# Kernel optimization log

Measured on AMD Instinct MI355X. Metric: run time of the kernel, lower is better.

The kernel has to match this reference:

```python
import jax, jax.numpy as jnp
import numpy as np

PAD = [(1, 1), (1, 1), (1, 1)]
DN = ('NCDHW', 'OIDHW', 'NCDHW')


def conv3d(x, w):
    # x: [B,Ci,D,H,W], w: [Co,Ci,3,3,3], stride 1, pad 1 (BasicConv3d, bn=False, bias=False)
    return jax.lax.conv_general_dilated(x, w, (1, 1, 1), PAD, dimension_numbers=DN)


def deconv3d(x, w):
    # torch ConvTranspose3d weight [Ci,Co,3,3,3], stride 1, pad 1 == conv with spatially flipped kernel
    wf = jnp.flip(w, axis=(2, 3, 4)).transpose(1, 0, 2, 3, 4)
    return conv3d(x, wf)


def sru_dir(X, Wx, F, R, reverse):
    # SRU linear recurrence over the spectral axis (dim 2).
    # t=0: C = 1 - f_0 (faithful to SRUconvLayer's Ct-is-None branch)
    # t>0: C = f*C + (1-f)*Wx ;  h = r*C + (1-r)*x
    mt = lambda a: jnp.moveaxis(a, 2, 0)  # [T,B,C,H,W]
    x, w, f, r = mt(X), mt(Wx), mt(F), mt(R)
    if reverse:
        x, w, f, r = x[::-1], w[::-1], f[::-1], r[::-1]
    C0 = 1.0 - f[0]
    h0 = r[0] * C0 + (1.0 - r[0]) * x[0]

    def step(C, inp):
        x_, w_, f_, r_ = inp
        Cn = f_ * C + (1.0 - f_) * w_
        return Cn, r_ * Cn + (1.0 - r_) * x_

    _, hs = jax.lax.scan(step, C0, (x[1:], w[1:], f[1:], r[1:]))
    h = jnp.concatenate([h0[None], hs], axis=0)
    if reverse:
        h = h[::-1]
    return jnp.moveaxis(h, 0, 2)


def do_sru(x, w, deconv=False):
    # DoSRUconv: 6-way gate split, bidirectional scan (ft/rt forward, ft2/rt2 backward), sum
    g = deconv3d(x, w) if deconv else conv3d(x, w)
    Wx, ft, ft2, rt, rt2, X = jnp.split(g, 6, axis=1)
    Wx = jnp.tanh(Wx)
    X = jnp.tanh(X)  # act == 'tanh'
    ft, ft2, rt, rt2 = (jax.nn.sigmoid(a) for a in (ft, ft2, rt, rt2))
    return sru_dir(X, Wx, ft, rt, False) + sru_dir(X, Wx, ft2, rt2, True)


def si_sru(x, w, reverse, deconv=False):
    # SiSRUconv: 4-way gate split, single-direction scan
    g = deconv3d(x, w) if deconv else conv3d(x, w)
    Wx, ft, rt, X = jnp.split(g, 4, axis=1)
    return sru_dir(jnp.tanh(X), jnp.tanh(Wx), jax.nn.sigmoid(ft), jax.nn.sigmoid(rt), reverse)


def nssnn_forward(x, w_head, w_e0, w_e1, w_d0, w_d1, w_tail):
    h = do_sru(x, w_head)                                 # head: 1 -> 16, bidirectional
    e0 = si_sru(h, w_e0, reverse=False)                   # encoder: 16 -> 32 (alt direction)
    e1 = si_sru(e0, w_e1, reverse=True)                   # encoder: 32 -> 64
    d0 = si_sru(e1, w_d0, reverse=False, deconv=True) + e0  # decoder: 64 -> 32, skip add
    d1 = si_sru(d0, w_d1, reverse=True, deconv=True) + h    # decoder: 32 -> 16, skip add
    out = do_sru(d1, w_tail, deconv=True)                 # tail: 16 -> 1, bidirectional
    return out + x                                        # global residual


def setup_inputs() -> dict:
    key = jax.random.key(0)
    ks = jax.random.split(key, 7)
    B, Cin, Ch, D, H, W = 1, 1, 16, 31, 96, 96
    s = 0.05
    x = jax.random.normal(ks[0], (B, Cin, D, H, W), dtype=jnp.float32)
    w_head = jax.random.normal(ks[1], (6 * Ch, Cin, 3, 3, 3), dtype=jnp.float32) * s
    w_e0 = jax.random.normal(ks[2], (4 * 2 * Ch, Ch, 3, 3, 3), dtype=jnp.float32) * s
    w_e1 = jax.random.normal(ks[3], (4 * 4 * Ch, 2 * Ch, 3, 3, 3), dtype=jnp.float32) * s
    # ConvTranspose3d weights: [Cin, Cout, 3,3,3]
    w_d0 = jax.random.normal(ks[4], (4 * Ch, 4 * 2 * Ch, 3, 3, 3), dtype=jnp.float32) * s
    w_d1 = jax.random.normal(ks[5], (2 * Ch, 4 * Ch, 3, 3, 3), dtype=jnp.float32) * s
    w_tail = jax.random.normal(ks[6], (Ch, 6 * Cin, 3, 3, 3), dtype=jnp.float32) * s
    return {"x": x, "w_head": w_head, "w_e0": w_e0, "w_e1": w_e1,
            "w_d0": w_d0, "w_d1": w_d1, "w_tail": w_tail}


def reference(x, w_head, w_e0, w_e1, w_d0, w_d1, w_tail):
    return nssnn_forward(x, w_head, w_e0, w_e1, w_d0, w_d1, w_tail)
```

## Files before the change

### kernel.cpp

```cpp
#include <hip/hip_runtime.h>
#include <hip/hip_bf16.h>


#define D_DIM 31
#define H_DIM 96
#define W_DIM 96
#define HW (H_DIM * W_DIM)
#define SVOX (D_DIM * HW)

typedef __hip_bfloat16 bf16;
typedef __attribute__((ext_vector_type(8))) short short8;
typedef __attribute__((ext_vector_type(4))) short short4a;
typedef __attribute__((ext_vector_type(4))) float f32x4;

__device__ __forceinline__ float sigm(float v) { return 1.0f / (1.0f + __expf(-v)); }
__device__ __forceinline__ short f2bs(float v) {
    bf16 h = __float2bfloat16(v);
    return *(short*)&h;
}
__device__ __forceinline__ float bs2f(short s) {
    return __uint_as_float(((unsigned)(unsigned short)s) << 16);
}

template <typename T> __device__ __forceinline__ float ldf(const T* p);
template <> __device__ __forceinline__ float ldf<float>(const float* p) { return *p; }
template <> __device__ __forceinline__ float ldf<bf16>(const bf16* p) {
    return __bfloat162float(*p);
}
template <typename T> __device__ __forceinline__ void stf(T* p, float v);
template <> __device__ __forceinline__ void stf<float>(float* p, float v) { *p = v; }
template <> __device__ __forceinline__ void stf<bf16>(bf16* p, float v) {
    *p = __float2bfloat16(v);
}

#define P8 ((size_t)8 * SVOX)

__global__ __launch_bounds__(256) void wtrans_all_k(const float* __restrict__ w_e0,
                                                    const float* __restrict__ w_e1,
                                                    const float* __restrict__ w_d0,
                                                    const float* __restrict__ w_d1,
                                                    bf16* __restrict__ wt) {
    int i = blockIdx.x * 256 + threadIdx.x;
    if (i >= 608256) return;
    const float* w;
    int j, C_in, C_out_w, Ch, deconv, cip;
    if (i < 110592)      { w = w_e0; j = i;          C_in = 16; C_out_w = 128; Ch = 32; deconv = 0; cip = 32; }
    else if (i < 331776) { w = w_e1; j = i - 110592; C_in = 32; C_out_w = 256; Ch = 64; deconv = 0; cip = 32; }
    else if (i < 552960) { w = w_d0; j = i - 331776; C_in = 64; C_out_w = 128; Ch = 32; deconv = 1; cip = 64; }
    else                 { w = w_d1; j = i - 552960; C_in = 32; C_out_w = 64;  Ch = 16; deconv = 1; cip = 32; }
    int ci = j % cip;
    int r = j / cip;
    int oc_c = r & 31; r >>= 5;
    int kk = r % 27;
    int chunk = r / 27;
    int oc_w = (oc_c >> 3) * Ch + chunk * 8 + (oc_c & 7);
    float v = 0.0f;
    if (ci < C_in)
        v = deconv ? w[((size_t)ci * C_out_w + oc_w) * 27 + (26 - kk)]
                   : w[((size_t)oc_w * C_in + ci) * 27 + kk];
    wt[i] = __float2bfloat16(v);
}

template <int CI32>
__global__ __launch_bounds__(256) void conv_mfma_k(const bf16* __restrict__ x,
                                                   const bf16* __restrict__ wt,
                                                   bf16* __restrict__ g, int C_in) {
    constexpr int RS = 40;
    constexpr int CIP = CI32 * 32;
    __shared__ short row[6 * 98 * RS];

    const int t = threadIdx.x;
    const int lane = t & 63, wave = t >> 6;
    const int l15 = lane & 15, g4 = lane >> 4;
    const int h0 = blockIdx.x * 4, d = blockIdx.y;
    const short* xs = (const short*)x;

    f32x4 acc[6][2];
#pragma unroll
    for (int m = 0; m < 6; ++m)
#pragma unroll
        for (int n = 0; n < 2; ++n) acc[m][n] = (f32x4){0.f, 0.f, 0.f, 0.f};

    for (int kd = 0; kd < 3; ++kd) {
        const int dd = d + kd - 1;
        if ((unsigned)dd >= D_DIM) continue;
        for (int cb = 0; cb < CI32; ++cb) {
            __syncthreads();
            for (int i = t; i < 98 * 6 * 4; i += 256) {
                int wp = i % 98;
                int j = i / 98;
                int hl = j % 6;
                int cg = j / 6;
                int hh = h0 + hl - 1;
                int gw = wp - 1;
                const int cblk = cb * 4 + cg;
                short8 v = {0, 0, 0, 0, 0, 0, 0, 0};
                if ((unsigned)hh < H_DIM && (unsigned)gw < W_DIM && cblk * 8 < C_in)
                    v = *(const short8*)(xs + (size_t)cblk * P8 +
                                         ((size_t)dd * HW + hh * W_DIM + gw) * 8);
                *(short8*)(row + ((size_t)hl * 98 + wp) * RS + cg * 8) = v;
            }
            __syncthreads();

            const bf16* wa = wt + (size_t)l15 * CIP + cb * 32 + g4 * 8;
#pragma unroll
            for (int kh = 0; kh < 3; ++kh) {
#pragma unroll
                for (int kw = 0; kw < 3; ++kw) {
                    const int kk = (kd * 3 + kh) * 3 + kw;
                    const size_t arow = (size_t)kk * 32 * CIP;
                    short8 a0 = *(const short8*)(wa + arow);
                    short8 a1 = *(const short8*)(wa + arow + (size_t)16 * CIP);
                    const int boff = ((wave + kh) * 98 + l15 + kw) * RS + g4 * 8;
#pragma unroll
                    for (int m = 0; m < 6; ++m) {
                        short8 b = *(const short8*)(row + boff + (m * 16) * RS);
                        acc[m][0] = __builtin_amdgcn_mfma_f32_16x16x32_bf16(a0, b, acc[m][0], 0, 0, 0);
                        acc[m][1] = __builtin_amdgcn_mfma_f32_16x16x32_bf16(a1, b, acc[m][1], 0, 0, 0);
                    }
                }
            }
        }
    }

    const int hy = h0 + wave;
    short* gs = (short*)g;
#pragma unroll
    for (int m = 0; m < 6; ++m) {
        const int wx = m * 16 + l15;
        const size_t dhw = (size_t)d * HW + hy * W_DIM + wx;
#pragma unroll
        for (int n = 0; n < 2; ++n) {
            const int gate = n * 2 + (g4 >> 1);
            const bool th = (gate == 0 || gate == 3);
            short4a pack;
#pragma unroll
            for (int r = 0; r < 4; ++r) {
                float a = acc[m][n][r];
                pack[r] = f2bs(th ? tanhf(a) : sigm(a));
            }
            *(short4a*)(gs + (size_t)gate * P8 + dhw * 8 + (g4 & 1) * 4) = pack;
        }
    }
}

__global__ __launch_bounds__(256) void head_conv_k(const float* __restrict__ x,
                                                   const float* __restrict__ w,
                                                   bf16* __restrict__ g, int c0) {
    __shared__ float tile[3][34][36];
    __shared__ float wsh[8 * 27];

    const int t = threadIdx.x;
    const int lx = t & 15;
    const int ly = t >> 4;
    const int tbx = (blockIdx.x % 3) * 32;
    const int tby = (blockIdx.x / 3) * 32;
    const int d = blockIdx.y;
    const int gidx = blockIdx.z;
    const int ocw0 = gidx * 16 + c0;

    if (t < 8 * 27) wsh[t] = w[(ocw0 + t / 27) * 27 + (t % 27)];

    for (int i = t; i < 3 * 34 * 34; i += 256) {
        int dz = i / 1156;
        int rem = i - dz * 1156;
        int r = rem / 34;
        int c = rem - r * 34;
        int gd = d + dz - 1;
        int gy = tby + r - 1;
        int gx = tbx + c - 1;
        float v = 0.0f;
        if ((unsigned)gd < D_DIM && (unsigned)gy < H_DIM && (unsigned)gx < W_DIM)
            v = x[((size_t)gd * H_DIM + gy) * W_DIM + gx];
        tile[dz][r][c] = v;
    }
    __syncthreads();

    float acc[8][4];
#pragma unroll
    for (int o = 0; o < 8; ++o)
#pragma unroll
        for (int p = 0; p < 4; ++p) acc[o][p] = 0.0f;

#pragma unroll
    for (int kd = 0; kd < 3; ++kd)
#pragma unroll
        for (int kh = 0; kh < 3; ++kh) {
            float wv[8][3];
#pragma unroll
            for (int o = 0; o < 8; ++o)
#pragma unroll
                for (int kw = 0; kw < 3; ++kw)
                    wv[o][kw] = wsh[o * 27 + (kd * 3 + kh) * 3 + kw];
            const int r0 = ly * 2 + kh;
            float v0[4], v1[4];
#pragma unroll
            for (int c = 0; c < 4; ++c) {
                v0[c] = tile[kd][r0][lx * 2 + c];
                v1[c] = tile[kd][r0 + 1][lx * 2 + c];
            }
#pragma unroll
            for (int kw = 0; kw < 3; ++kw)
#pragma unroll
                for (int o = 0; o < 8; ++o) {
                    acc[o][0] = fmaf(v0[kw],     wv[o][kw], acc[o][0]);
                    acc[o][1] = fmaf(v0[kw + 1], wv[o][kw], acc[o][1]);
                    acc[o][2] = fmaf(v1[kw],     wv[o][kw], acc[o][2]);
                    acc[o][3] = fmaf(v1[kw + 1], wv[o][kw], acc[o][3]);
                }
        }

    const bool th = (gidx == 0 || gidx == 5);
    const int hy = tby + ly * 2, wx = tbx + lx * 2;
    short* gs = (short*)g;
#pragma unroll
    for (int p = 0; p < 4; ++p) {
        const int py = hy + (p >> 1), px = wx + (p & 1);
        short8 pack;
#pragma unroll
        for (int o = 0; o < 8; ++o) {
            float a = acc[o][p];
            pack[o] = f2bs(th ? tanhf(a) : sigm(a));
        }
        *(short8*)(gs + (size_t)gidx * P8 + ((size_t)d * HW + py * W_DIM + px) * 8) = pack;
    }
}

__global__ __launch_bounds__(256) void tail_conv_k(const bf16* __restrict__ x,
                                                   const float* __restrict__ w,
                                                   bf16* __restrict__ g) {
    __shared__ short tile[3][18][18][8];
    __shared__ float wsh[8 * 6 * 27];

    const int t = threadIdx.x;
    const int lx = t & 15;
    const int ly = t >> 4;
    const int tbx = (blockIdx.x % 6) * 16;
    const int tby = (blockIdx.x / 6) * 16;
    const int d = blockIdx.y;
    const short* xs = (const short*)x;

    float acc[6] = {0.f, 0.f, 0.f, 0.f, 0.f, 0.f};

    for (int cb = 0; cb < 2; ++cb) {
        __syncthreads();
        for (int i = t; i < 8 * 6 * 27; i += 256) {
            int u = i / 162, rem = i % 162, o = rem / 27, k = rem % 27;
            wsh[i] = w[((cb * 8 + u) * 6 + o) * 27 + (26 - k)];
        }
        for (int i = t; i < 3 * 18 * 18; i += 256) {
            int dz = i / 324;
            int rem = i % 324;
            int r = rem / 18;
            int cc = rem % 18;
            int gd = d + dz - 1;
            int gy = tby + r - 1;
            int gx = tbx + cc - 1;
            short8 v = {0, 0, 0, 0, 0, 0, 0, 0};
            if ((unsigned)gd < D_DIM && (unsigned)gy < H_DIM && (unsigned)gx < W_DIM)
                v = *(const short8*)(xs + (size_t)cb * P8 +
                                     ((size_t)gd * HW + gy * W_DIM + gx) * 8);
            *(short8*)&tile[dz][r][cc][0] = v;
        }
        __syncthreads();

#pragma unroll
        for (int kd = 0; kd < 3; ++kd)
#pragma unroll
            for (int kh = 0; kh < 3; ++kh)
#pragma unroll
                for (int kw = 0; kw < 3; ++kw) {
                    short8 tv = *(short8*)&tile[kd][ly + kh][lx + kw][0];
                    const int k = (kd * 3 + kh) * 3 + kw;
#pragma unroll
                    for (int u = 0; u < 8; ++u) {
                        float xv = bs2f(tv[u]);
#pragma unroll
                        for (int o = 0; o < 6; ++o)
                            acc[o] = fmaf(xv, wsh[(u * 6 + o) * 27 + k], acc[o]);
                    }
                }
    }

    const size_t dhw = (size_t)d * HW + (tby + ly) * W_DIM + (tbx + lx);
#pragma unroll
    for (int o = 0; o < 6; ++o) {
        const bool th = (o == 0 || o == 5);
        stf(g + (size_t)o * SVOX + dhw, th ? tanhf(acc[o]) : sigm(acc[o]));
    }
}

template <int REV>
__global__ __launch_bounds__(256) void si_sru_scan_k(const bf16* __restrict__ g,
                                                     const bf16* __restrict__ resid,
                                                     bf16* __restrict__ out, int outblk) {
    const int idx = blockIdx.x * 256 + threadIdx.x;
    const int c = idx & 7;
    const size_t hw = (size_t)(idx >> 3);

    const bf16* oW = g;
    const bf16* oF = g + P8;
    const bf16* oR = g + 2 * P8;
    const bf16* oX = g + 3 * P8;
    const size_t ob = (size_t)outblk * P8;

    float C = 0.0f;
#pragma unroll
    for (int i = 0; i < D_DIM; ++i) {
        const int d = REV ? (D_DIM - 1 - i) : i;
        const size_t off = ((size_t)d * HW + hw) * 8 + c;
        float f = ldf(oF + off);
        float r = ldf(oR + off);
        float xv = ldf(oX + off);
        float wv = ldf(oW + off);
        C = (i == 0) ? (1.0f - f) : (f * C + (1.0f - f) * wv);
        float hv = r * C + (1.0f - r) * xv;
        float o = hv + (resid ? ldf(resid + ob + off) : 0.0f);
        stf(out + ob + off, o);
    }
}

__global__ __launch_bounds__(256) void do_sru_scan_k(const bf16* __restrict__ g,
                                                     bf16* __restrict__ out, int outblk) {
    const int idx = blockIdx.x * 256 + threadIdx.x;
    const int c = idx & 7;
    const size_t hw = (size_t)(idx >> 3);
    const size_t ob = (size_t)outblk * P8;

    float hbuf[D_DIM];
    float C = 0.0f;
#pragma unroll
    for (int d = 0; d < D_DIM; ++d) {
        const size_t off = ((size_t)d * HW + hw) * 8 + c;
        float f = ldf(g + P8 + off);
        float r = ldf(g + 3 * P8 + off);
        float xv = ldf(g + 5 * P8 + off);
        float wv = ldf(g + off);
        C = (d == 0) ? (1.0f - f) : (f * C + (1.0f - f) * wv);
        hbuf[d] = r * C + (1.0f - r) * xv;
    }
#pragma unroll
    for (int i = 0; i < D_DIM; ++i) {
        const int d = D_DIM - 1 - i;
        const size_t off = ((size_t)d * HW + hw) * 8 + c;
        float f = ldf(g + 2 * P8 + off);
        float r = ldf(g + 4 * P8 + off);
        float xv = ldf(g + 5 * P8 + off);
        float wv = ldf(g + off);
        C = (i == 0) ? (1.0f - f) : (f * C + (1.0f - f) * wv);
        hbuf[d] += r * C + (1.0f - r) * xv;
    }
#pragma unroll
    for (int d = 0; d < D_DIM; ++d)
        stf(out + ob + ((size_t)d * HW + hw) * 8 + c, hbuf[d]);
}

__global__ __launch_bounds__(256) void do_sru_final_k(const bf16* __restrict__ g,
                                                      const float* __restrict__ x,
                                                      float* __restrict__ out) {
    const size_t hw = (size_t)(blockIdx.x * 256 + threadIdx.x);

    float hbuf[D_DIM];
    float C = 0.0f;
#pragma unroll
    for (int d = 0; d < D_DIM; ++d) {
        const size_t off = (size_t)d * HW + hw;
        float f = ldf(g + SVOX + off);
        float r = ldf(g + 3 * (size_t)SVOX + off);
        float xv = ldf(g + 5 * (size_t)SVOX + off);
        float wv = ldf(g + off);
        C = (d == 0) ? (1.0f - f) : (f * C + (1.0f - f) * wv);
        hbuf[d] = r * C + (1.0f - r) * xv;
    }
#pragma unroll
    for (int i = 0; i < D_DIM; ++i) {
        const int d = D_DIM - 1 - i;
        const size_t off = (size_t)d * HW + hw;
        float f = ldf(g + 2 * (size_t)SVOX + off);
        float r = ldf(g + 4 * (size_t)SVOX + off);
        float xv = ldf(g + 5 * (size_t)SVOX + off);
        float wv = ldf(g + off);
        C = (i == 0) ? (1.0f - f) : (f * C + (1.0f - f) * wv);
        hbuf[d] += r * C + (1.0f - r) * xv + x[off];
    }
#pragma unroll
    for (int d = 0; d < D_DIM; ++d) out[(size_t)d * HW + hw] = hbuf[d];
}

extern "C" void kernel_launch(void* const* d_in, const int* in_sizes, int n_in,
                              void* d_out, int out_size, void* d_ws, size_t ws_size,
                              hipStream_t stream) {
    const float* x      = (const float*)d_in[0];
    const float* w_head = (const float*)d_in[1];
    const float* w_e0   = (const float*)d_in[2];
    const float* w_e1   = (const float*)d_in[3];
    const float* w_d0   = (const float*)d_in[4];
    const float* w_d1   = (const float*)d_in[5];
    const float* w_tail = (const float*)d_in[6];
    float* out = (float*)d_out;

    bf16* g  = (bf16*)d_ws;
    bf16* wt = g + (size_t)32 * SVOX;
    bf16* H  = g + (size_t)48 * SVOX;
    bf16* E0 = H + (size_t)16 * SVOX;
    bf16* E1 = E0 + (size_t)32 * SVOX;
    bf16* D0 = E0;
    bf16* D1 = E1;

    dim3 blk(256);
    const dim3 sg8(8 * 36);
    const dim3 mg(H_DIM / 4, D_DIM);

    for (int c0 = 0; c0 < 16; c0 += 8) {
        head_conv_k<<<dim3(9, 31, 6), blk, 0, stream>>>(x, w_head, g, c0);
        do_sru_scan_k<<<sg8, blk, 0, stream>>>(g, H, c0 >> 3);
    }
    wtrans_all_k<<<dim3((608256 + 255) / 256), blk, 0, stream>>>(w_e0, w_e1, w_d0, w_d1, wt);

    for (int c = 0; c < 4; ++c) {
        conv_mfma_k<1><<<mg, blk, 0, stream>>>(H, wt + (size_t)c * 27648, g, 16);
        si_sru_scan_k<0><<<sg8, blk, 0, stream>>>(g, (const bf16*)nullptr, E0, c);
    }
    for (int c = 0; c < 8; ++c) {
        conv_mfma_k<1><<<mg, blk, 0, stream>>>(E0, wt + 110592 + (size_t)c * 27648, g, 32);
        si_sru_scan_k<1><<<sg8, blk, 0, stream>>>(g, (const bf16*)nullptr, E1, c);
    }
    for (int c = 0; c < 4; ++c) {
        conv_mfma_k<2><<<mg, blk, 0, stream>>>(E1, wt + 331776 + (size_t)c * 55296, g, 64);
        si_sru_scan_k<0><<<sg8, blk, 0, stream>>>(g, E0, D0, c);
    }
    for (int c = 0; c < 2; ++c) {
        conv_mfma_k<1><<<mg, blk, 0, stream>>>(D0, wt + 552960 + (size_t)c * 27648, g, 32);
        si_sru_scan_k<1><<<sg8, blk, 0, stream>>>(g, H, D1, c);
    }
    tail_conv_k<<<dim3(36, 31), blk, 0, stream>>>(D1, w_tail, g);
    do_sru_final_k<<<dim3(36), blk, 0, stream>>>(g, x, out);
}
```

Before: 1.293 ms.

## Route tail conv through MFMA kernel, batch head conv/scan, pad LDS rows

Replaces the scalar FMA tail convolution with the MFMA conv kernel, templated on tile count and epilogue, using a pre-transposed flipped tail weight block added to the weight transform. Head conv and bidirectional scan now run once over all 16 channels instead of two launches each, which needs a reworked workspace layout. LDS row stride drops from 40 to 34 shorts to cut bank conflicts, though short8 loads at that stride may lose 16-byte alignment. The tail MFMA path wastes most of its output tile because only 6 of 16 channels are real.

```diff
diff --git a/kernel.cpp b/kernel.cpp
--- a/kernel.cpp
+++ b/kernel.cpp
@@ -39,9 +39,22 @@
                                                     const float* __restrict__ w_e1,
                                                     const float* __restrict__ w_d0,
                                                     const float* __restrict__ w_d1,
+                                                    const float* __restrict__ w_tail,
                                                     bf16* __restrict__ wt) {
     int i = blockIdx.x * 256 + threadIdx.x;
-    if (i >= 608256) return;
+    if (i >= 635904) return;
+    if (i >= 608256) {
+        int j = i - 608256;
+        int ci = j % 32;
+        int r = j / 32;
+        int oc_c = r & 31;
+        int kk = (r >> 5) % 27;
+        float v = 0.0f;
+        if (ci < 16 && oc_c < 6)
+            v = w_tail[(ci * 6 + oc_c) * 27 + (26 - kk)];
+        wt[i] = __float2bfloat16(v);
+        return;
+    }
     const float* w;
     int j, C_in, C_out_w, Ch, deconv, cip;
     if (i < 110592)      { w = w_e0; j = i;          C_in = 16; C_out_w = 128; Ch = 32; deconv = 0; cip = 32; }
@@ -61,11 +74,11 @@
     wt[i] = __float2bfloat16(v);
 }
 
-template <int CI32>
+template <int CI32, int NT, int EPI>
 __global__ __launch_bounds__(256) void conv_mfma_k(const bf16* __restrict__ x,
                                                    const bf16* __restrict__ wt,
                                                    bf16* __restrict__ g, int C_in) {
-    constexpr int RS = 40;
+    constexpr int RS = 34;
     constexpr int CIP = CI32 * 32;
     __shared__ short row[6 * 98 * RS];
 
@@ -75,11 +88,11 @@
     const int h0 = blockIdx.x * 4, d = blockIdx.y;
     const short* xs = (const short*)x;
 
-    f32x4 acc[6][2];
+    f32x4 acc[6][NT];
 #pragma unroll
     for (int m = 0; m < 6; ++m)
 #pragma unroll
-        for (int n = 0; n < 2; ++n) acc[m][n] = (f32x4){0.f, 0.f, 0.f, 0.f};
+        for (int n = 0; n < NT; ++n) acc[m][n] = (f32x4){0.f, 0.f, 0.f, 0.f};
 
     for (int kd = 0; kd < 3; ++kd) {
         const int dd = d + kd - 1;
@@ -110,13 +123,15 @@
                     const int kk = (kd * 3 + kh) * 3 + kw;
                     const size_t arow = (size_t)kk * 32 * CIP;
                     short8 a0 = *(const short8*)(wa + arow);
-                    short8 a1 = *(const short8*)(wa + arow + (size_t)16 * CIP);
+                    short8 a1;
+                    if (NT == 2) a1 = *(const short8*)(wa + arow + (size_t)16 * CIP);
                     const int boff = ((wave + kh) * 98 + l15 + kw) * RS + g4 * 8;
 #pragma unroll
                     for (int m = 0; m < 6; ++m) {
                         short8 b = *(const short8*)(row + boff + (m * 16) * RS);
                         acc[m][0] = __builtin_amdgcn_mfma_f32_16x16x32_bf16(a0, b, acc[m][0], 0, 0, 0);
-                        acc[m][1] = __builtin_amdgcn_mfma_f32_16x16x32_bf16(a1, b, acc[m][1], 0, 0, 0);
+                        if (NT == 2)
+                            acc[m][1] = __builtin_amdgcn_mfma_f32_16x16x32_bf16(a1, b, acc[m][1], 0, 0, 0);
                     }
                 }
             }
@@ -129,24 +144,36 @@
     for (int m = 0; m < 6; ++m) {
         const int wx = m * 16 + l15;
         const size_t dhw = (size_t)d * HW + hy * W_DIM + wx;
-#pragma unroll
-        for (int n = 0; n < 2; ++n) {
-            const int gate = n * 2 + (g4 >> 1);
-            const bool th = (gate == 0 || gate == 3);
-            short4a pack;
+        if (EPI == 0) {
+#pragma unroll
+            for (int n = 0; n < NT; ++n) {
+                const int gate = n * 2 + (g4 >> 1);
+                const bool th = (gate == 0 || gate == 3);
+                short4a pack;
+#pragma unroll
+                for (int r = 0; r < 4; ++r) {
+                    float a = acc[m][n][r];
+                    pack[r] = f2bs(th ? tanhf(a) : sigm(a));
+                }
+                *(short4a*)(gs + (size_t)gate * P8 + dhw * 8 + (g4 & 1) * 4) = pack;
+            }
+        } else {
 #pragma unroll
             for (int r = 0; r < 4; ++r) {
-                float a = acc[m][n][r];
-                pack[r] = f2bs(th ? tanhf(a) : sigm(a));
-            }
-            *(short4a*)(gs + (size_t)gate * P8 + dhw * 8 + (g4 & 1) * 4) = pack;
+                const int oc = g4 * 4 + r;
+                if (oc < 6) {
+                    float a = acc[m][0][r];
+                    const bool th = (oc == 0 || oc == 5);
+                    stf(g + (size_t)oc * SVOX + dhw, th ? tanhf(a) : sigm(a));
+                }
+            }
         }
     }
 }
 
 __global__ __launch_bounds__(256) void head_conv_k(const float* __restrict__ x,
                                                    const float* __restrict__ w,
-                                                   bf16* __restrict__ g, int c0) {
+                                                   bf16* __restrict__ g) {
     __shared__ float tile[3][34][36];
     __shared__ float wsh[8 * 27];
 
@@ -156,8 +183,9 @@
     const int tbx = (blockIdx.x % 3) * 32;
     const int tby = (blockIdx.x / 3) * 32;
     const int d = blockIdx.y;
-    const int gidx = blockIdx.z;
-    const int ocw0 = gidx * 16 + c0;
+    const int bz = blockIdx.z;
+    const int gate = bz >> 1;
+    const int ocw0 = gate * 16 + (bz & 1) * 8;
 
     if (t < 8 * 27) wsh[t] = w[(ocw0 + t / 27) * 27 + (t % 27)];
 
@@ -210,7 +238,7 @@
                 }
         }
 
-    const bool th = (gidx == 0 || gidx == 5);
+    const bool th = (gate == 0 || gate == 5);
     const int hy = tby + ly * 2, wx = tbx + lx * 2;
     short* gs = (short*)g;
 #pragma unroll
@@ -222,71 +250,7 @@
             float a = acc[o][p];
             pack[o] = f2bs(th ? tanhf(a) : sigm(a));
         }
-        *(short8*)(gs + (size_t)gidx * P8 + ((size_t)d * HW + py * W_DIM + px) * 8) = pack;
-    }
-}
-
-__global__ __launch_bounds__(256) void tail_conv_k(const bf16* __restrict__ x,
-                                                   const float* __restrict__ w,
-                                                   bf16* __restrict__ g) {
-    __shared__ short tile[3][18][18][8];
-    __shared__ float wsh[8 * 6 * 27];
-
-    const int t = threadIdx.x;
-    const int lx = t & 15;
-    const int ly = t >> 4;
-    const int tbx = (blockIdx.x % 6) * 16;
-    const int tby = (blockIdx.x / 6) * 16;
-    const int d = blockIdx.y;
-    const short* xs = (const short*)x;
-
-    float acc[6] = {0.f, 0.f, 0.f, 0.f, 0.f, 0.f};
-
-    for (int cb = 0; cb < 2; ++cb) {
-        __syncthreads();
-        for (int i = t; i < 8 * 6 * 27; i += 256) {
-            int u = i / 162, rem = i % 162, o = rem / 27, k = rem % 27;
-            wsh[i] = w[((cb * 8 + u) * 6 + o) * 27 + (26 - k)];
-        }
-        for (int i = t; i < 3 * 18 * 18; i += 256) {
-            int dz = i / 324;
-            int rem = i % 324;
-            int r = rem / 18;
-            int cc = rem % 18;
-            int gd = d + dz - 1;
-            int gy = tby + r - 1;
-            int gx = tbx + cc - 1;
-            short8 v = {0, 0, 0, 0, 0, 0, 0, 0};
-            if ((unsigned)gd < D_DIM && (unsigned)gy < H_DIM && (unsigned)gx < W_DIM)
-                v = *(const short8*)(xs + (size_t)cb * P8 +
-                                     ((size_t)gd * HW + gy * W_DIM + gx) * 8);
-            *(short8*)&tile[dz][r][cc][0] = v;
-        }
-        __syncthreads();
-
-#pragma unroll
-        for (int kd = 0; kd < 3; ++kd)
-#pragma unroll
-            for (int kh = 0; kh < 3; ++kh)
-#pragma unroll
-                for (int kw = 0; kw < 3; ++kw) {
-                    short8 tv = *(short8*)&tile[kd][ly + kh][lx + kw][0];
-                    const int k = (kd * 3 + kh) * 3 + kw;
-#pragma unroll
-                    for (int u = 0; u < 8; ++u) {
-                        float xv = bs2f(tv[u]);
-#pragma unroll
-                        for (int o = 0; o < 6; ++o)
-                            acc[o] = fmaf(xv, wsh[(u * 6 + o) * 27 + k], acc[o]);
-                    }
-                }
-    }
-
-    const size_t dhw = (size_t)d * HW + (tby + ly) * W_DIM + (tbx + lx);
-#pragma unroll
-    for (int o = 0; o < 6; ++o) {
-        const bool th = (o == 0 || o == 5);
-        stf(g + (size_t)o * SVOX + dhw, th ? tanhf(acc[o]) : sigm(acc[o]));
+        *(short8*)(gs + (size_t)bz * P8 + ((size_t)d * HW + py * W_DIM + px) * 8) = pack;
     }
 }
 
@@ -297,11 +261,6 @@
     const int idx = blockIdx.x * 256 + threadIdx.x;
     const int c = idx & 7;
     const size_t hw = (size_t)(idx >> 3);
-
-    const bf16* oW = g;
-    const bf16* oF = g + P8;
-    const bf16* oR = g + 2 * P8;
-    const bf16* oX = g + 3 * P8;
     const size_t ob = (size_t)outblk * P8;
 
     float C = 0.0f;
@@ -309,10 +268,10 @@
     for (int i = 0; i < D_DIM; ++i) {
         const int d = REV ? (D_DIM - 1 - i) : i;
         const size_t off = ((size_t)d * HW + hw) * 8 + c;
-        float f = ldf(oF + off);
-        float r = ldf(oR + off);
-        float xv = ldf(oX + off);
-        float wv = ldf(oW + off);
+        float f = ldf(g + P8 + off);
+        float r = ldf(g + 2 * P8 + off);
+        float xv = ldf(g + 3 * P8 + off);
+        float wv = ldf(g + off);
         C = (i == 0) ? (1.0f - f) : (f * C + (1.0f - f) * wv);
         float hv = r * C + (1.0f - r) * xv;
         float o = hv + (resid ? ldf(resid + ob + off) : 0.0f);
@@ -321,21 +280,22 @@
 }
 
 __global__ __launch_bounds__(256) void do_sru_scan_k(const bf16* __restrict__ g,
-                                                     bf16* __restrict__ out, int outblk) {
-    const int idx = blockIdx.x * 256 + threadIdx.x;
-    const int c = idx & 7;
-    const size_t hw = (size_t)(idx >> 3);
-    const size_t ob = (size_t)outblk * P8;
+                                                     bf16* __restrict__ out) {
+    const int j = blockIdx.x * 256 + threadIdx.x;
+    const int c = j & 7;
+    const size_t hw = (size_t)(j >> 3);
+    const int chb = blockIdx.y;
+    const bf16* gb = g + (size_t)chb * P8;
 
     float hbuf[D_DIM];
     float C = 0.0f;
 #pragma unroll
     for (int d = 0; d < D_DIM; ++d) {
         const size_t off = ((size_t)d * HW + hw) * 8 + c;
-        float f = ldf(g + P8 + off);
-        float r = ldf(g + 3 * P8 + off);
-        float xv = ldf(g + 5 * P8 + off);
-        float wv = ldf(g + off);
+        float f = ldf(gb + 2 * P8 + off);
+        float r = ldf(gb + 6 * P8 + off);
+        float xv = ldf(gb + 10 * P8 + off);
+        float wv = ldf(gb + off);
         C = (d == 0) ? (1.0f - f) : (f * C + (1.0f - f) * wv);
         hbuf[d] = r * C + (1.0f - r) * xv;
     }
@@ -343,16 +303,16 @@
     for (int i = 0; i < D_DIM; ++i) {
         const int d = D_DIM - 1 - i;
         const size_t off = ((size_t)d * HW + hw) * 8 + c;
-        float f = ldf(g + 2 * P8 + off);
-        float r = ldf(g + 4 * P8 + off);
-        float xv = ldf(g + 5 * P8 + off);
-        float wv = ldf(g + off);
+        float f = ldf(gb + 4 * P8 + off);
+        float r = ldf(gb + 8 * P8 + off);
+        float xv = ldf(gb + 10 * P8 + off);
+        float wv = ldf(gb + off);
         C = (i == 0) ? (1.0f - f) : (f * C + (1.0f - f) * wv);
         hbuf[d] += r * C + (1.0f - r) * xv;
     }
 #pragma unroll
     for (int d = 0; d < D_DIM; ++d)
-        stf(out + ob + ((size_t)d * HW + hw) * 8 + c, hbuf[d]);
+        stf(out + (size_t)chb * P8 + ((size_t)d * HW + hw) * 8 + c, hbuf[d]);
 }
 
 __global__ __launch_bounds__(256) void do_sru_final_k(const bf16* __restrict__ g,
@@ -401,9 +361,9 @@
 
     bf16* g  = (bf16*)d_ws;
     bf16* wt = g + (size_t)32 * SVOX;
-    bf16* H  = g + (size_t)48 * SVOX;
-    bf16* E0 = H + (size_t)16 * SVOX;
-    bf16* E1 = E0 + (size_t)32 * SVOX;
+    bf16* E1 = g + (size_t)48 * SVOX;
+    bf16* E0 = g + (size_t)112 * SVOX;
+    bf16* H  = g + (size_t)144 * SVOX;
     bf16* D0 = E0;
     bf16* D1 = E1;
 
@@ -411,28 +371,26 @@
     const dim3 sg8(8 * 36);
     const dim3 mg(H_DIM / 4, D_DIM);
 
-    for (int c0 = 0; c0 < 16; c0 += 8) {
-        head_conv_k<<<dim3(9, 31, 6), blk, 0, stream>>>(x, w_head, g, c0);
-        do_sru_scan_k<<<sg8, blk, 0, stream>>>(g, H, c0 >> 3);
-    }
-    wtrans_all_k<<<dim3((608256 + 255) / 256), blk, 0, stream>>>(w_e0, w_e1, w_d0, w_d1, wt);
+    head_conv_k<<<dim3(9, 31, 12), blk, 0, stream>>>(x, w_head, g);
+    do_sru_scan_k<<<dim3(288, 2), blk, 0, stream>>>(g, H);
+    wtrans_all_k<<<dim3((635904 + 255) / 256), blk, 0, stream>>>(w_e0, w_e1, w_d0, w_d1, w_tail, wt);
 
     for (int c = 0; c < 4; ++c) {
-        conv_mfma_k<1><<<mg, blk, 0, stream>>>(H, wt + (size_t)c * 27648, g, 16);
+        conv_mfma_k<1, 2, 0><<<mg, blk, 0, stream>>>(H, wt + (size_t)c * 27648, g, 16);
         si_sru_scan_k<0><<<sg8, blk, 0, stream>>>(g, (const bf16*)nullptr, E0, c);
     }
     for (int c = 0; c < 8; ++c) {
-        conv_mfma_k<1><<<mg, blk, 0, stream>>>(E0, wt + 110592 + (size_t)c * 27648, g, 32);
+        conv_mfma_k<1, 2, 0><<<mg, blk, 0, stream>>>(E0, wt + 110592 + (size_t)c * 27648, g, 32);
         si_sru_scan_k<1><<<sg8, blk, 0, stream>>>(g, (const bf16*)nullptr, E1, c);
     }
     for (int c = 0; c < 4; ++c) {
-        conv_mfma_k<2><<<mg, blk, 0, stream>>>(E1, wt + 331776 + (size_t)c * 55296, g, 64);
+        conv_mfma_k<2, 2, 0><<<mg, blk, 0, stream>>>(E1, wt + 331776 + (size_t)c * 55296, g, 64);
         si_sru_scan_k<0><<<sg8, blk, 0, stream>>>(g, E0, D0, c);
     }
     for (int c = 0; c < 2; ++c) {
-        conv_mfma_k<1><<<mg, blk, 0, stream>>>(D0, wt + 552960 + (size_t)c * 27648, g, 32);
+        conv_mfma_k<1, 2, 0><<<mg, blk, 0, stream>>>(D0, wt + 552960 + (size_t)c * 27648, g, 32);
         si_sru_scan_k<1><<<sg8, blk, 0, stream>>>(g, H, D1, c);
     }
-    tail_conv_k<<<dim3(36, 31), blk, 0, stream>>>(D1, w_tail, g);
+    conv_mfma_k<1, 1, 1><<<mg, blk, 0, stream>>>(D1, wt + 608256, g, 16);
     do_sru_final_k<<<dim3(36), blk, 0, stream>>>(g, x, out);
 }
```

Measured after the change: 1.295 ms. Within noise of the previous version (+0.1%).
